# Performance work log

Hardware: AMD Instinct MI355X
Metric: run time of the kernel (lower is better)

Reference implementation:

```python
import jax, jax.numpy as jnp
import numpy as np

N = 20000          # nodes
E = 320000         # edges
D_IN = 128         # input_dim
HGC = 64           # hidden per gconv layer
LG = 4             # number of ChebConv layers
K = 4              # Chebyshev order (hardcoded)
NUM_CLASSES = 2
HID_BYS = 16       # bayesian hidden_dim (hardcoded)
NSAMP = 25         # 5 outer x 5 inner chained sampling iterations
BN_SCALE = 1.0 / np.sqrt(1.0 + 1e-5)  # eval BatchNorm with default running stats
COS_EPS = 1e-8


def setup_inputs() -> dict:
    key = jax.random.key(0)
    ks = jax.random.split(key, 16)
    f32 = jnp.float32
    d = {}
    d["features"] = jax.random.normal(ks[0], (N, D_IN), f32)
    d["edge_index"] = jax.random.randint(ks[1], (2, E), 0, N)
    d["edgenet_input"] = jax.random.normal(ks[2], (E, 128), f32)
    half = 64  # edgenet_input_dim // 2
    # associationP MLP: Linear(64,512) ReLU BN Linear(512,256) ReLU BN Drop Linear(256,128)
    d["We1"] = jax.random.normal(ks[3], (512, half), f32) * np.sqrt(2.0 / half)
    d["be1"] = jnp.zeros((512,), f32)
    d["We2"] = jax.random.normal(ks[4], (256, 512), f32) * np.sqrt(2.0 / 512)
    d["be2"] = jnp.zeros((256,), f32)
    d["We3"] = jax.random.normal(ks[5], (128, 256), f32) * np.sqrt(2.0 / 256)
    d["be3"] = jnp.zeros((128,), f32)
    # ChebConv weights, [K, in, out], no bias
    d["cheb_w0"] = jax.random.normal(ks[6], (K, D_IN, HGC), f32) * np.sqrt(2.0 / D_IN)
    d["cheb_w1"] = jax.random.normal(ks[7], (K, HGC, HGC), f32) * np.sqrt(2.0 / HGC)
    d["cheb_w2"] = jax.random.normal(ks[8], (K, HGC, HGC), f32) * np.sqrt(2.0 / HGC)
    d["cheb_w3"] = jax.random.normal(ks[9], (K, HGC, HGC), f32) * np.sqrt(2.0 / HGC)
    cls_in = HGC * LG  # 256, jumping-knowledge concat
    d["Wm1"] = jax.random.normal(ks[10], (256, cls_in), f32) * np.sqrt(2.0 / cls_in)
    d["bm1"] = jnp.zeros((256,), f32)
    d["Wm2"] = jax.random.normal(ks[11], (NUM_CLASSES, 256), f32) * np.sqrt(2.0 / 256)
    d["bm2"] = jnp.zeros((NUM_CLASSES,), f32)
    d["Wl"] = jax.random.normal(ks[12], (HID_BYS, D_IN), f32) * np.sqrt(2.0 / D_IN)
    d["bl"] = jnp.zeros((HID_BYS,), f32)
    hl_in = NSAMP * HID_BYS  # 400, the freshly-created Linear2
    d["Whl"] = jax.random.normal(ks[13], (NUM_CLASSES, hl_in), f32) * np.sqrt(1.0 / hl_in)
    d["bhl"] = jnp.zeros((NUM_CLASSES,), f32)
    # prior Normal(0,1) samples, one per node per sampling iteration
    d["noise"] = jax.random.normal(ks[14], (NSAMP, N, HID_BYS), f32)
    return d


def _edge_mlp(x, We1, be1, We2, be2, We3, be3):
    h = jax.nn.relu(x @ We1.T + be1) * BN_SCALE
    h = jax.nn.relu(h @ We2.T + be2) * BN_SCALE
    return h @ We3.T + be3


def _forward(features, edge_index, edgenet_input, We1, be1, We2, be2, We3, be3,
             cheb_w0, cheb_w1, cheb_w2, cheb_w3, Wm1, bm1, Wm2, bm2,
             Wl, bl, Whl, bhl, noise):
    row, col = edge_index[0], edge_index[1]

    # ---- edge weights via associationP (cosine similarity head) ----
    h1 = _edge_mlp(edgenet_input[:, :64], We1, be1, We2, be2, We3, be3)
    h2 = _edge_mlp(edgenet_input[:, 64:], We1, be1, We2, be2, We3, be3)
    n1 = jnp.maximum(jnp.sqrt(jnp.sum(h1 * h1, -1)), COS_EPS)
    n2 = jnp.maximum(jnp.sqrt(jnp.sum(h2 * h2, -1)), COS_EPS)
    cos = jnp.sum(h1 * h2, -1) / (n1 * n2)
    ew = (cos + 1.0) * 0.5  # [E]

    # ---- ChebConv sym-normalized scaled Laplacian (lambda_max=2 -> zero diag) ----
    w = jnp.where(row == col, 0.0, ew)  # remove_self_loops
    deg = jax.ops.segment_sum(w, row, num_segments=N)
    dinv = jnp.where(deg > 0, jax.lax.rsqrt(deg), 0.0)
    lapw = -dinv[row] * w * dinv[col]  # L_hat off-diagonal weights

    def prop(x):  # L_hat @ x  (diag is exactly 0)
        return jax.ops.segment_sum(lapw[:, None] * x[row], col, num_segments=N)

    def cheb(x, W):  # W: [K, in, out]
        tx0, tx1 = x, prop(x)
        out = tx0 @ W[0] + tx1 @ W[1]
        for k in range(2, K):
            tx2 = 2.0 * prop(tx1) - tx0
            out = out + tx2 @ W[k]
            tx0, tx1 = tx1, tx2
        return out

    # ---- dense_gcn branch with jumping-knowledge concat ----
    h = jax.nn.relu(cheb(features, cheb_w0))
    jk = h
    for W in (cheb_w1, cheb_w2, cheb_w3):
        h = jax.nn.relu(cheb(h, W))
        jk = jnp.concatenate([jk, h], axis=1)
    m = jax.nn.relu(jk @ Wm1.T + bm1) * BN_SCALE
    logit1 = m @ Wm2.T + bm2  # [N, C]

    # ---- bys_gcn branch: 25 chained iterations h <- noise + scatter_add(w*h[src]) ----
    h0 = features @ Wl.T + bl  # [N, 16]

    def step(hc, nz):
        agg = jax.ops.segment_sum(ew[:, None] * hc[row], col, num_segments=N)
        hn = nz + agg
        return hn, hn

    _, states = jax.lax.scan(step, h0, noise)  # [25, N, 16]
    # faithful to torch .view(N, -1) on the [5,5,N,16] stack (row-major reshape)
    feats2 = states.reshape(N, NSAMP * HID_BYS)  # [N, 400]
    logit2 = jax.nn.sigmoid(feats2 @ Whl.T + bhl)  # [N, C]

    p1 = jax.nn.softmax(logit1, axis=1)
    p2 = jax.nn.softmax(logit2, axis=1)
    return p1, p2, jnp.maximum(p1, p2)


def reference(features, edge_index, edgenet_input, We1, be1, We2, be2, We3, be3,
              cheb_w0, cheb_w1, cheb_w2, cheb_w3, Wm1, bm1, Wm2, bm2,
              Wl, bl, Whl, bhl, noise):
    return _forward(features, edge_index, edgenet_input, We1, be1, We2, be2, We3, be3,
                    cheb_w0, cheb_w1, cheb_w2, cheb_w3, Wm1, bm1, Wm2, bm2,
                    Wl, bl, Whl, bhl, noise)
```

## Files before the change

kernel.cpp:

```cpp
#include <hip/hip_runtime.h>
#include <math.h>

#define NN 20000
#define EE 320000
#define BN_SC 0.9999950000374997f

typedef __attribute__((ext_vector_type(8))) short bf16x8;
typedef __attribute__((ext_vector_type(4))) float f32x4;

__device__ __forceinline__ unsigned short f2b(float x) {
  unsigned int u = __builtin_bit_cast(unsigned int, x);
  u += 0x7FFFu + ((u >> 16) & 1u);
  return (unsigned short)(u >> 16);
}
__device__ __forceinline__ void split2(float x, unsigned short& h, unsigned short& l) {
  h = f2b(x);
  float hf = __builtin_bit_cast(float, (unsigned int)h << 16);
  l = f2b(x - hf);
}

__global__ __launch_bounds__(256) void k_wpack(const float* __restrict__ W, unsigned short* __restrict__ Wh,
                                               unsigned short* __restrict__ Wl, int C, int K) {
  int i = blockIdx.x * 256 + threadIdx.x;
  if (i >= C * K) return;
  int e = i & 7;
  int lane = (i >> 3) & 63;
  int tile = i >> 9;
  int KT = K >> 5;
  int kt = tile % KT, ct = tile / KT;
  int lr = lane & 15, lg = lane >> 4;
  int col = ct * 16 + lr;
  int k = kt * 32 + lg * 8 + e;
  unsigned short h, l;
  split2(W[(size_t)col * K + k], h, l);
  Wh[i] = h;
  Wl[i] = l;
}

__global__ __launch_bounds__(256) void k_count(const int* __restrict__ colv, int* __restrict__ cnt) {
  int e = blockIdx.x * 256 + threadIdx.x;
  if (e < EE) atomicAdd(&cnt[colv[e]], 1);
}

__global__ __launch_bounds__(256) void k_scan1(const int* __restrict__ cnt, int* __restrict__ offs,
                                               int* __restrict__ bsum) {
  __shared__ int sb[256];
  int t = threadIdx.x, i = blockIdx.x * 256 + t;
  int v = (i < NN) ? cnt[i] : 0;
  sb[t] = v;
  __syncthreads();
  for (int off = 1; off < 256; off <<= 1) {
    int x = (t >= off) ? sb[t - off] : 0;
    __syncthreads();
    sb[t] += x;
    __syncthreads();
  }
  if (i < NN) offs[i + 1] = sb[t];
  if (t == 255) bsum[blockIdx.x] = sb[255];
}
__global__ __launch_bounds__(128) void k_scan2(int* __restrict__ bsum) {
  __shared__ int sb[128];
  int t = threadIdx.x;
  int v = (t < 79) ? bsum[t] : 0;
  sb[t] = v;
  __syncthreads();
  for (int off = 1; off < 128; off <<= 1) {
    int x = (t >= off) ? sb[t - off] : 0;
    __syncthreads();
    sb[t] += x;
    __syncthreads();
  }
  if (t < 79) bsum[t] = sb[t] - v;
}
__global__ __launch_bounds__(256) void k_scan3(const int* __restrict__ bsum, int* __restrict__ offs) {
  int i = blockIdx.x * 256 + threadIdx.x;
  if (i == 0) offs[0] = 0;
  if (i < NN) offs[i + 1] += bsum[blockIdx.x];
}

__global__ __launch_bounds__(256) void k_fill(const int* __restrict__ colv, const int* __restrict__ offs,
                                              int* __restrict__ cur, int* __restrict__ eid) {
  int e = blockIdx.x * 256 + threadIdx.x;
  if (e < EE) {
    int d = colv[e];
    int p = atomicAdd(&cur[d], 1);
    eid[offs[d] + p] = e;
  }
}

__global__ __launch_bounds__(64) void k_sortl(const int* __restrict__ offs, int* __restrict__ eid) {
  __shared__ int buf[64 * 97];
  int n = blockIdx.x * 64 + threadIdx.x;
  if (n >= NN) return;
  int j0 = offs[n], j1 = offs[n + 1], d = j1 - j0;
  int* b = &buf[threadIdx.x * 97];
  if (d <= 96) {
    for (int i = 0; i < d; ++i) b[i] = eid[j0 + i];
    for (int i = 1; i < d; ++i) {
      int v = b[i];
      int j = i - 1;
      while (j >= 0 && b[j] > v) { b[j + 1] = b[j]; --j; }
      b[j + 1] = v;
    }
    for (int i = 0; i < d; ++i) eid[j0 + i] = b[i];
  } else {
    for (int i = j0 + 1; i < j1; ++i) {
      int v = eid[i];
      int j = i - 1;
      while (j >= j0 && eid[j] > v) { eid[j + 1] = eid[j]; --j; }
      eid[j + 1] = v;
    }
  }
}

__global__ __launch_bounds__(256) void k_pack(const int* __restrict__ eid, const int* __restrict__ rowi,
                                              const int* __restrict__ colv,
                                              const float* __restrict__ ew, const float* __restrict__ dinv,
                                              float2* __restrict__ packW, float2* __restrict__ packL) {
  int j = blockIdx.x * 256 + threadIdx.x;
  if (j < EE) {
    int e = eid[j];
    int r = rowi[e], c = colv[e];
    float rw = __int_as_float(r);
    float w = (r == c) ? 0.f : ew[e];
    packW[j] = make_float2(ew[e], rw);
    packL[j] = make_float2(-dinv[r] * w * dinv[c], rw);
  }
}

#define MFMA16(a, b, c) __builtin_amdgcn_mfma_f32_16x16x32_bf16(a, b, c, 0, 0, 0)

__global__ __launch_bounds__(512, 2) void k_edge_mlp(
    const float* __restrict__ X,
    const unsigned short* __restrict__ W1h, const unsigned short* __restrict__ W1l, const float* __restrict__ b1,
    const unsigned short* __restrict__ W2h, const unsigned short* __restrict__ W2l, const float* __restrict__ b2,
    const unsigned short* __restrict__ W3h, const unsigned short* __restrict__ W3l, const float* __restrict__ b3,
    float* __restrict__ ew) {
  __shared__ __align__(16) unsigned short POOL[24576];
  unsigned short* Xh = POOL;
  unsigned short* Xl = POOL + 4096;
  unsigned short* H2ch = POOL + 8192;
  unsigned short* H2cl = POOL + 16384;
  float* H3 = (float*)(POOL + 8192);

  const int tid = threadIdx.x;
  const int wv = tid >> 6;
  const int lane = tid & 63;
  const int lr = lane & 15;
  const int lg = lane >> 4;
  const int e0 = blockIdx.x * 32;
  const int lane8 = lane << 3;

  const int rt1 = wv & 3;
  const int ch1 = wv >> 2;

  {
    int row = tid >> 3, eighth = tid & 7;
    const float* src = X + (size_t)(e0 + (row >> 1)) * 128 + (row & 1) * 64 + eighth * 8;
    float4 a = ((const float4*)src)[0];
    float4 b = ((const float4*)src)[1];
    float vals[8] = {a.x, a.y, a.z, a.w, b.x, b.y, b.z, b.w};
    unsigned short hs[8], ls[8];
#pragma unroll
    for (int j = 0; j < 8; ++j) split2(vals[j], hs[j], ls[j]);
    int chunk = eighth ^ (row & 7);
    int idxs = row * 64 + chunk * 8;
#pragma unroll
    for (int j = 0; j < 8; ++j) { Xh[idxs + j] = hs[j]; Xl[idxs + j] = ls[j]; }
  }
  __syncthreads();

  auto l1_compute = [&](int c, int b) {
    unsigned short* H1h = POOL + 8192 + b * 8192;
    unsigned short* H1l = POOL + 12288 + b * 8192;
    f32x4 acc1[2];
#pragma unroll
    for (int cti = 0; cti < 2; ++cti) acc1[cti] = f32x4{0.f, 0.f, 0.f, 0.f};
#pragma unroll
    for (int kt = 0; kt < 2; ++kt) {
      int arow = 16 * rt1 + lr;
      int aidx = arow * 64 + ((4 * kt + lg) ^ (arow & 7)) * 8;
      bf16x8 ah = *(const bf16x8*)&Xh[aidx];
      bf16x8 al = *(const bf16x8*)&Xl[aidx];
#pragma unroll
      for (int cti = 0; cti < 2; ++cti) {
        int off = (((4 * c + 2 * ch1 + cti) * 2 + kt) << 9) + lane8;
        bf16x8 bh = *(const bf16x8*)(W1h + off);
        bf16x8 bl = *(const bf16x8*)(W1l + off);
        acc1[cti] = MFMA16(ah, bh, acc1[cti]);
        acc1[cti] = MFMA16(ah, bl, acc1[cti]);
        acc1[cti] = MFMA16(al, bh, acc1[cti]);
      }
    }
#pragma unroll
    for (int cti = 0; cti < 2; ++cti) {
      int colL = 16 * (2 * ch1 + cti) + lr;
      float bias = b1[64 * c + colL];
#pragma unroll
      for (int r = 0; r < 4; ++r) {
        float v = fmaxf(acc1[cti][r] + bias, 0.f) * BN_SC;
        unsigned short hs, ls;
        split2(v, hs, ls);
        int row = 16 * rt1 + 4 * lg + r;
        int idxs = row * 64 + (((colL >> 3) ^ (row & 7)) * 8) + (colL & 7);
        H1h[idxs] = hs;
        H1l[idxs] = ls;
      }
    }
  };

  f32x4 acc2[4][2];
#pragma unroll
  for (int rt = 0; rt < 4; ++rt)
#pragma unroll
    for (int ct = 0; ct < 2; ++ct) acc2[rt][ct] = f32x4{0.f, 0.f, 0.f, 0.f};

  l1_compute(0, 0);
  __syncthreads();

  for (int kc = 0; kc < 8; ++kc) {
    int cur = kc & 1;
    unsigned short* H1h = POOL + 8192 + cur * 8192;
    unsigned short* H1l = POOL + 12288 + cur * 8192;
    bf16x8 p2h[2], p2l[2];
    {
#pragma unroll
      for (int ct = 0; ct < 2; ++ct) {
        int off = (((8 * ct + wv) * 16 + 2 * kc) << 9) + lane8;
        p2h[ct] = *(const bf16x8*)(W2h + off);
        p2l[ct] = *(const bf16x8*)(W2l + off);
      }
    }
    if (kc < 7) l1_compute(kc + 1, cur ^ 1);
    bf16x8 q2h[2], q2l[2];
    {
#pragma unroll
      for (int ct = 0; ct < 2; ++ct) {
        int off = (((8 * ct + wv) * 16 + 2 * kc + 1) << 9) + lane8;
        q2h[ct] = *(const bf16x8*)(W2h + off);
        q2l[ct] = *(const bf16x8*)(W2l + off);
      }
    }
#pragma unroll
    for (int rtg = 0; rtg < 2; ++rtg) {
      bf16x8 ah[2], al[2];
#pragma unroll
      for (int rti = 0; rti < 2; ++rti) {
        int arow = 32 * rtg + 16 * rti + lr;
        int aidx = arow * 64 + (lg ^ (arow & 7)) * 8;
        ah[rti] = *(const bf16x8*)&H1h[aidx];
        al[rti] = *(const bf16x8*)&H1l[aidx];
      }
#pragma unroll
      for (int ct = 0; ct < 2; ++ct)
#pragma unroll
        for (int rti = 0; rti < 2; ++rti) {
          acc2[2 * rtg + rti][ct] = MFMA16(ah[rti], p2h[ct], acc2[2 * rtg + rti][ct]);
          acc2[2 * rtg + rti][ct] = MFMA16(ah[rti], p2l[ct], acc2[2 * rtg + rti][ct]);
          acc2[2 * rtg + rti][ct] = MFMA16(al[rti], p2h[ct], acc2[2 * rtg + rti][ct]);
        }
    }
#pragma unroll
    for (int rtg = 0; rtg < 2; ++rtg) {
      bf16x8 ah[2], al[2];
#pragma unroll
      for (int rti = 0; rti < 2; ++rti) {
        int arow = 32 * rtg + 16 * rti + lr;
        int aidx = arow * 64 + ((4 + lg) ^ (arow & 7)) * 8;
        ah[rti] = *(const bf16x8*)&H1h[aidx];
        al[rti] = *(const bf16x8*)&H1l[aidx];
      }
#pragma unroll
      for (int ct = 0; ct < 2; ++ct)
#pragma unroll
        for (int rti = 0; rti < 2; ++rti) {
          acc2[2 * rtg + rti][ct] = MFMA16(ah[rti], q2h[ct], acc2[2 * rtg + rti][ct]);
          acc2[2 * rtg + rti][ct] = MFMA16(ah[rti], q2l[ct], acc2[2 * rtg + rti][ct]);
          acc2[2 * rtg + rti][ct] = MFMA16(al[rti], q2h[ct], acc2[2 * rtg + rti][ct]);
        }
    }
    __syncthreads();
  }

  f32x4 acc3[4];
#pragma unroll
  for (int rt = 0; rt < 4; ++rt) acc3[rt] = f32x4{0.f, 0.f, 0.f, 0.f};
  const int w3col = 16 * wv + lr;

#pragma unroll
  for (int ch = 0; ch < 2; ++ch) {
    bf16x8 w3h_c, w3l_c;
    {
      int off = ((wv * 8 + 4 * ch) << 9) + lane8;
      w3h_c = *(const bf16x8*)(W3h + off);
      w3l_c = *(const bf16x8*)(W3l + off);
    }
    if (ch) __syncthreads();
    {
      int colC = 16 * wv + lr;
      float bias = b2[128 * ch + colC];
#pragma unroll
      for (int rt = 0; rt < 4; ++rt) {
#pragma unroll
        for (int r = 0; r < 4; ++r) {
          float v = fmaxf(acc2[rt][ch][r] + bias, 0.f) * BN_SC;
          unsigned short hs, ls;
          split2(v, hs, ls);
          int row = 16 * rt + 4 * lg + r;
          int idxs = row * 128 + (((colC >> 3) ^ (row & 7)) * 8) + (colC & 7);
          H2ch[idxs] = hs;
          H2cl[idxs] = ls;
        }
      }
    }
    __syncthreads();
#pragma unroll
    for (int kt = 0; kt < 4; ++kt) {
      bf16x8 w3h_n, w3l_n;
      if (kt < 3) {
        int off = ((wv * 8 + 4 * ch + kt + 1) << 9) + lane8;
        w3h_n = *(const bf16x8*)(W3h + off);
        w3l_n = *(const bf16x8*)(W3l + off);
      }
#pragma unroll
      for (int rtg = 0; rtg < 2; ++rtg) {
        bf16x8 ah[2], al[2];
#pragma unroll
        for (int rti = 0; rti < 2; ++rti) {
          int arow = 32 * rtg + 16 * rti + lr;
          int aidx = arow * 128 + (((4 * kt + lg) ^ (arow & 7)) * 8);
          ah[rti] = *(const bf16x8*)&H2ch[aidx];
          al[rti] = *(const bf16x8*)&H2cl[aidx];
        }
#pragma unroll
        for (int rti = 0; rti < 2; ++rti) {
          acc3[2 * rtg + rti] = MFMA16(ah[rti], w3h_c, acc3[2 * rtg + rti]);
          acc3[2 * rtg + rti] = MFMA16(ah[rti], w3l_c, acc3[2 * rtg + rti]);
          acc3[2 * rtg + rti] = MFMA16(al[rti], w3h_c, acc3[2 * rtg + rti]);
        }
      }
      w3h_c = w3h_n;
      w3l_c = w3l_n;
    }
  }
  __syncthreads();

  {
    float bias = b3[w3col];
#pragma unroll
    for (int rt = 0; rt < 4; ++rt)
#pragma unroll
      for (int r = 0; r < 4; ++r)
        H3[(16 * rt + 4 * lg + r) * 128 + w3col] = acc3[rt][r] + bias;
  }
  __syncthreads();

  {
    int i = tid >> 4, j = tid & 15;
    const float* ra = &H3[(2 * i) * 128];
    const float* rb = &H3[(2 * i + 1) * 128];
    float dot = 0.f, s1 = 0.f, s2 = 0.f;
#pragma unroll
    for (int s = 0; s < 8; ++s) {
      float a = ra[j + 16 * s], b = rb[j + 16 * s];
      dot += a * b;
      s1 += a * a;
      s2 += b * b;
    }
#pragma unroll
    for (int m = 8; m >= 1; m >>= 1) {
      dot += __shfl_xor(dot, m);
      s1 += __shfl_xor(s1, m);
      s2 += __shfl_xor(s2, m);
    }
    if (j == 0) {
      float n1 = fmaxf(sqrtf(s1), 1e-8f);
      float n2 = fmaxf(sqrtf(s2), 1e-8f);
      float cosv = dot / (n1 * n2);
      ew[e0 + i] = (cosv + 1.f) * 0.5f;
    }
  }
}

__global__ __launch_bounds__(256) void k_deg(const int* __restrict__ rowi, const int* __restrict__ colv,
                                             const float* __restrict__ ew, float* __restrict__ deg) {
  int e = blockIdx.x * 256 + threadIdx.x;
  if (e < EE) {
    int r = rowi[e];
    float w = (r == colv[e]) ? 0.f : ew[e];
    atomicAdd(&deg[r], w);
  }
}
__global__ __launch_bounds__(256) void k_dinv(const float* __restrict__ deg, float* __restrict__ dinv) {
  int n = blockIdx.x * 256 + threadIdx.x;
  if (n < NN) { float d = deg[n]; dinv[n] = d > 0.f ? 1.f / sqrtf(d) : 0.f; }
}

template <int DIM>
__global__ __launch_bounds__(256) void k_prop(const float* __restrict__ x, int ldx,
                                              const float* __restrict__ y, int ldy,
                                              float alpha, float beta,
                                              float* __restrict__ outv, int ldo,
                                              const float2* __restrict__ packL,
                                              const int* __restrict__ offs) {
  constexpr int FG = DIM / 4;
  int idx = blockIdx.x * 256 + threadIdx.x;
  int n = idx / FG, g = (idx % FG) * 4;
  if (n >= NN) return;
  float ax = 0.f, ay = 0.f, az = 0.f, aw = 0.f;
  int j1 = offs[n + 1];
  for (int j = offs[n]; j < j1; ++j) {
    float2 p = packL[j];
    float4 v = *(const float4*)(x + (size_t)__float_as_int(p.y) * ldx + g);
    ax += p.x * v.x; ay += p.x * v.y; az += p.x * v.z; aw += p.x * v.w;
  }
  float4 r = make_float4(alpha * ax, alpha * ay, alpha * az, alpha * aw);
  if (beta != 0.f) {
    float4 yv = *(const float4*)(y + (size_t)n * ldy + g);
    r.x += beta * yv.x; r.y += beta * yv.y; r.z += beta * yv.z; r.w += beta * yv.w;
  }
  *(float4*)(outv + (size_t)n * ldo + g) = r;
}

template <int DK>
__global__ __launch_bounds__(512) void k_combine(const float* __restrict__ t0, int ld0,
                                                 const float* __restrict__ t1, int ld1,
                                                 const float* __restrict__ t2, int ld2,
                                                 const float* __restrict__ t3, int ld3,
                                                 const float* __restrict__ W,
                                                 float* __restrict__ outp) {
  int n = blockIdx.x * 8 + (threadIdx.x >> 6);
  int c = threadIdx.x & 63;
  if (n >= NN) return;
  const float* r0 = t0 + (size_t)n * ld0;
  const float* r1 = t1 + (size_t)n * ld1;
  const float* r2 = t2 + (size_t)n * ld2;
  const float* r3 = t3 + (size_t)n * ld3;
  const float* w0 = W;
  const float* w1 = W + DK * 64;
  const float* w2 = W + 2 * DK * 64;
  const float* w3 = W + 3 * DK * 64;
  float acc = 0.f;
#pragma unroll 4
  for (int d = 0; d < DK; ++d) {
    acc += r0[d] * w0[d * 64 + c];
    acc += r1[d] * w1[d * 64 + c];
    acc += r2[d] * w2[d * 64 + c];
    acc += r3[d] * w3[d * 64 + c];
  }
  outp[(size_t)n * 256 + c] = fmaxf(acc, 0.f);
}

__global__ void k_tr256(const float* __restrict__ A, float* __restrict__ At) {
  int c = blockIdx.x, k = threadIdx.x;
  At[(size_t)k * 256 + c] = A[(size_t)c * 256 + k];
}

__global__ __launch_bounds__(256) void k_mlogit(const float* __restrict__ jk, const float* __restrict__ Wm1t,
                                                const float* __restrict__ bm1, const float* __restrict__ Wm2,
                                                const float* __restrict__ bm2, float* __restrict__ logit1) {
  __shared__ float jks[16 * 256];
  __shared__ float red[16 * 8];
  int tid = threadIdx.x, n0 = blockIdx.x * 16;
  {
    const float4* src = (const float4*)(jk + (size_t)n0 * 256);
    float4* dst = (float4*)jks;
#pragma unroll
    for (int u = 0; u < 4; ++u) dst[tid + 256 * u] = src[tid + 256 * u];
  }
  __syncthreads();
  int c = tid;
  float acc[16];
  float bb = bm1[c];
#pragma unroll
  for (int r = 0; r < 16; ++r) acc[r] = bb;
  for (int k = 0; k < 256; k += 4) {
    float w0 = Wm1t[(size_t)(k + 0) * 256 + c];
    float w1 = Wm1t[(size_t)(k + 1) * 256 + c];
    float w2 = Wm1t[(size_t)(k + 2) * 256 + c];
    float w3 = Wm1t[(size_t)(k + 3) * 256 + c];
#pragma unroll
    for (int r = 0; r < 16; ++r) {
      float4 jv = *(const float4*)&jks[r * 256 + k];
      acc[r] += jv.x * w0 + jv.y * w1 + jv.z * w2 + jv.w * w3;
    }
  }
  float w20 = Wm2[c], w21 = Wm2[256 + c];
  int wid = tid >> 6, lane = tid & 63;
#pragma unroll
  for (int r = 0; r < 16; ++r) {
    float mv = fmaxf(acc[r], 0.f) * BN_SC;
    float v0 = mv * w20, v1 = mv * w21;
#pragma unroll
    for (int m = 32; m >= 1; m >>= 1) {
      v0 += __shfl_xor(v0, m, 64);
      v1 += __shfl_xor(v1, m, 64);
    }
    if (lane == 0) { red[r * 8 + wid] = v0; red[r * 8 + 4 + wid] = v1; }
  }
  __syncthreads();
  if (tid < 32) {
    int r = tid >> 1, cls = tid & 1;
    float s = red[r * 8 + cls * 4] + red[r * 8 + cls * 4 + 1] + red[r * 8 + cls * 4 + 2] + red[r * 8 + cls * 4 + 3];
    logit1[(size_t)(n0 + r) * 2 + cls] = s + bm2[cls];
  }
}

__global__ __launch_bounds__(256) void k_h0(const float* __restrict__ feat, const float* __restrict__ Wl,
                                            const float* __restrict__ bl, float* __restrict__ h0) {
  int idx = blockIdx.x * 256 + threadIdx.x;
  if (idx >= NN * 16) return;
  int n = idx >> 4, j = idx & 15;
  const float* fr = feat + (size_t)n * 128;
  const float* wr = Wl + (size_t)j * 128;
  float acc = bl[j];
#pragma unroll 8
  for (int d = 0; d < 128; d += 4) {
    float4 f = *(const float4*)(fr + d);
    float4 w = *(const float4*)(wr + d);
    acc += f.x * w.x + f.y * w.y + f.z * w.z + f.w * w.w;
  }
  h0[idx] = acc;
}

__global__ __launch_bounds__(256) void k_bys(const float* __restrict__ hprev, const float* __restrict__ nz,
                                             float* __restrict__ hout,
                                             const float2* __restrict__ packW,
                                             const int* __restrict__ offs) {
  int idx = blockIdx.x * 256 + threadIdx.x;
  int n = idx >> 2, g = (idx & 3) * 4;
  if (n >= NN) return;
  float ax = 0.f, ay = 0.f, az = 0.f, aw = 0.f;
  int j1 = offs[n + 1];
  for (int j = offs[n]; j < j1; ++j) {
    float2 p = packW[j];
    float4 v = *(const float4*)(hprev + ((size_t)__float_as_int(p.y) << 4) + g);
    ax += p.x * v.x; ay += p.x * v.y; az += p.x * v.z; aw += p.x * v.w;
  }
  float4 nv = *(const float4*)(nz + ((size_t)n << 4) + g);
  *(float4*)(hout + ((size_t)n << 4) + g) = make_float4(nv.x + ax, nv.y + ay, nv.z + az, nv.w + aw);
}

__global__ __launch_bounds__(256) void k_final(const float* __restrict__ states, const float* __restrict__ Whl,
                                               const float* __restrict__ bhl, const float* __restrict__ logit1,
                                               float* __restrict__ outp) {
  int n = blockIdx.x * 4 + (threadIdx.x >> 6);
  int l = threadIdx.x & 63;
  if (n >= NN) return;
  const float* sf = states + (size_t)n * 400;
  float a0 = 0.f, a1 = 0.f;
  for (int t = l; t < 400; t += 64) {
    float v = sf[t];
    a0 += v * Whl[t];
    a1 += v * Whl[400 + t];
  }
#pragma unroll
  for (int m = 32; m >= 1; m >>= 1) {
    a0 += __shfl_xor(a0, m, 64);
    a1 += __shfl_xor(a1, m, 64);
  }
  if (l == 0) {
    float z0 = 1.f / (1.f + expf(-(a0 + bhl[0])));
    float z1 = 1.f / (1.f + expf(-(a1 + bhl[1])));
    float p20 = 1.f / (1.f + expf(z1 - z0));
    float p21 = 1.f - p20;
    float l10 = logit1[(size_t)n * 2], l11 = logit1[(size_t)n * 2 + 1];
    float p10 = 1.f / (1.f + expf(l11 - l10));
    float p11 = 1.f - p10;
    outp[(size_t)n * 2] = p10;
    outp[(size_t)n * 2 + 1] = p11;
    outp[2 * NN + (size_t)n * 2] = p20;
    outp[2 * NN + (size_t)n * 2 + 1] = p21;
    outp[4 * NN + (size_t)n * 2] = fmaxf(p10, p20);
    outp[4 * NN + (size_t)n * 2 + 1] = fmaxf(p11, p21);
  }
}

extern "C" void kernel_launch(void* const* d_in, const int* in_sizes, int n_in,
                              void* d_out, int out_size, void* d_ws, size_t ws_size,
                              hipStream_t stream) {
  const float* feat = (const float*)d_in[0];
  const int* ei = (const int*)d_in[1];
  const float* xen = (const float*)d_in[2];
  const float* We1 = (const float*)d_in[3];
  const float* be1 = (const float*)d_in[4];
  const float* We2 = (const float*)d_in[5];
  const float* be2 = (const float*)d_in[6];
  const float* We3 = (const float*)d_in[7];
  const float* be3 = (const float*)d_in[8];
  const float* cw[4] = {(const float*)d_in[9], (const float*)d_in[10], (const float*)d_in[11], (const float*)d_in[12]};
  const float* Wm1 = (const float*)d_in[13];
  const float* bm1 = (const float*)d_in[14];
  const float* Wm2 = (const float*)d_in[15];
  const float* bm2 = (const float*)d_in[16];
  const float* Wl = (const float*)d_in[17];
  const float* bl = (const float*)d_in[18];
  const float* Whl = (const float*)d_in[19];
  const float* bhl = (const float*)d_in[20];
  const float* noise = (const float*)d_in[21];
  float* outp = (float*)d_out;

  char* wp_ = (char*)d_ws;
  auto alloc = [&](size_t bytes) {
    char* p = wp_;
    wp_ += (bytes + 255) & ~(size_t)255;
    return p;
  };
  float* ew = (float*)alloc((size_t)EE * 4);
  float* deg = (float*)alloc((size_t)NN * 4);
  float* dinv = (float*)alloc((size_t)NN * 4);
  int* cnt = (int*)alloc((size_t)NN * 4);
  int* offs = (int*)alloc((size_t)(NN + 1) * 4);
  int* bsum = (int*)alloc((size_t)128 * 4);
  int* eid = (int*)alloc((size_t)EE * 4);
  float2* packW = (float2*)alloc((size_t)EE * 8);
  float2* packL = (float2*)alloc((size_t)EE * 8);
  float* tx1 = (float*)alloc((size_t)NN * 128 * 4);
  float* tx2 = (float*)alloc((size_t)NN * 128 * 4);
  float* tx3 = (float*)alloc((size_t)NN * 128 * 4);
  float* jk = (float*)alloc((size_t)NN * 256 * 4);
  float* logit1 = (float*)alloc((size_t)NN * 2 * 4);
  float* Wm1t = (float*)alloc((size_t)256 * 256 * 4);
  float* h0 = (float*)alloc((size_t)NN * 16 * 4);
  float* states = (float*)alloc((size_t)25 * NN * 16 * 4);
  unsigned short* W1h = (unsigned short*)alloc((size_t)32768 * 2);
  unsigned short* W1l = (unsigned short*)alloc((size_t)32768 * 2);
  unsigned short* W2h = (unsigned short*)alloc((size_t)131072 * 2);
  unsigned short* W2l = (unsigned short*)alloc((size_t)131072 * 2);
  unsigned short* W3h = (unsigned short*)alloc((size_t)32768 * 2);
  unsigned short* W3l = (unsigned short*)alloc((size_t)32768 * 2);

  const int* rowi = ei;
  const int* colv = ei + EE;

  k_wpack<<<128, 256, 0, stream>>>(We1, W1h, W1l, 512, 64);
  k_wpack<<<512, 256, 0, stream>>>(We2, W2h, W2l, 256, 512);
  k_wpack<<<128, 256, 0, stream>>>(We3, W3h, W3l, 128, 256);

  hipMemsetAsync(cnt, 0, (size_t)NN * 4, stream);
  hipMemsetAsync(deg, 0, (size_t)NN * 4, stream);
  k_count<<<1250, 256, 0, stream>>>(colv, cnt);
  k_scan1<<<79, 256, 0, stream>>>(cnt, offs, bsum);
  k_scan2<<<1, 128, 0, stream>>>(bsum);
  k_scan3<<<79, 256, 0, stream>>>(bsum, offs);
  hipMemsetAsync(cnt, 0, (size_t)NN * 4, stream);
  k_fill<<<1250, 256, 0, stream>>>(colv, offs, cnt, eid);
  k_sortl<<<313, 64, 0, stream>>>(offs, eid);

  k_edge_mlp<<<10000, 512, 0, stream>>>(xen, W1h, W1l, be1, W2h, W2l, be2, W3h, W3l, be3, ew);

  k_deg<<<1250, 256, 0, stream>>>(rowi, colv, ew, deg);
  k_dinv<<<79, 256, 0, stream>>>(deg, dinv);
  k_pack<<<1250, 256, 0, stream>>>(eid, rowi, colv, ew, dinv, packW, packL);
  k_tr256<<<256, 256, 0, stream>>>(Wm1, Wm1t);

  k_prop<128><<<2500, 256, 0, stream>>>(feat, 128, feat, 128, 1.f, 0.f, tx1, 128, packL, offs);
  k_prop<128><<<2500, 256, 0, stream>>>(tx1, 128, feat, 128, 2.f, -1.f, tx2, 128, packL, offs);
  k_prop<128><<<2500, 256, 0, stream>>>(tx2, 128, tx1, 128, 2.f, -1.f, tx3, 128, packL, offs);
  k_combine<128><<<2500, 512, 0, stream>>>(feat, 128, tx1, 128, tx2, 128, tx3, 128, cw[0], jk);
  for (int l = 1; l < 4; ++l) {
    const float* xin = jk + (l - 1) * 64;
    k_prop<64><<<1250, 256, 0, stream>>>(xin, 256, xin, 256, 1.f, 0.f, tx1, 64, packL, offs);
    k_prop<64><<<1250, 256, 0, stream>>>(tx1, 64, xin, 256, 2.f, -1.f, tx2, 64, packL, offs);
    k_prop<64><<<1250, 256, 0, stream>>>(tx2, 64, tx1, 64, 2.f, -1.f, tx3, 64, packL, offs);
    k_combine<64><<<2500, 512, 0, stream>>>(xin, 256, tx1, 64, tx2, 64, tx3, 64, cw[l], jk + l * 64);
  }
  k_mlogit<<<1250, 256, 0, stream>>>(jk, Wm1t, bm1, Wm2, bm2, logit1);

  k_h0<<<1250, 256, 0, stream>>>(feat, Wl, bl, h0);
  const float* hprev = h0;
  for (int s = 0; s < 25; ++s) {
    float* hout = states + (size_t)s * NN * 16;
    k_bys<<<313, 256, 0, stream>>>(hprev, noise + (size_t)s * NN * 16, hout, packW, offs);
    hprev = hout;
  }
  k_final<<<5000, 256, 0, stream>>>(states, Whl, bhl, logit1, outp);
}
```

Before: 1.812 ms.

## Fuse h0 projection and 25 bys propagation steps into one persistent kernel with grid barriers

The 26 separate launches (the h0 projection plus 25 chained scatter steps) are replaced by one persistent kernel of 313 blocks that computes h0 and then loops over the 25 steps, separated by a software grid barrier built from atomics and threadfences. The aim is to remove per-launch overhead and the idle gaps between the small dependent launches. The h0 computation is rewritten so that each thread produces 4 outputs instead of 1. This relies on all 313 blocks being co-resident, otherwise the barrier deadlocks. Each step now pays for the barrier's atomic traffic and fences.

Result: slower. 3.553 ms (+96.1%).

```diff
diff --git a/kernel.cpp b/kernel.cpp
--- a/kernel.cpp
+++ b/kernel.cpp
@@ -4,6 +4,7 @@
 #define NN 20000
 #define EE 320000
 #define BN_SC 0.9999950000374997f
+#define BYS_NB 313
 
 typedef __attribute__((ext_vector_type(8))) short bf16x8;
 typedef __attribute__((ext_vector_type(4))) float f32x4;
@@ -506,39 +507,64 @@
   }
 }
 
-__global__ __launch_bounds__(256) void k_h0(const float* __restrict__ feat, const float* __restrict__ Wl,
-                                            const float* __restrict__ bl, float* __restrict__ h0) {
-  int idx = blockIdx.x * 256 + threadIdx.x;
-  if (idx >= NN * 16) return;
-  int n = idx >> 4, j = idx & 15;
-  const float* fr = feat + (size_t)n * 128;
-  const float* wr = Wl + (size_t)j * 128;
-  float acc = bl[j];
-#pragma unroll 8
-  for (int d = 0; d < 128; d += 4) {
-    float4 f = *(const float4*)(fr + d);
-    float4 w = *(const float4*)(wr + d);
-    acc += f.x * w.x + f.y * w.y + f.z * w.z + f.w * w.w;
-  }
-  h0[idx] = acc;
-}
-
-__global__ __launch_bounds__(256) void k_bys(const float* __restrict__ hprev, const float* __restrict__ nz,
-                                             float* __restrict__ hout,
-                                             const float2* __restrict__ packW,
-                                             const int* __restrict__ offs) {
+__device__ __forceinline__ void gridbar(int* __restrict__ bar, int nb) {
+  __threadfence();
+  __syncthreads();
+  if (threadIdx.x == 0) {
+    int g = atomicAdd(bar + 1, 0);
+    if (atomicAdd(bar, 1) == nb - 1) {
+      atomicExch(bar, 0);
+      __threadfence();
+      atomicAdd(bar + 1, 1);
+    } else {
+      while (atomicAdd(bar + 1, 0) == g) __builtin_amdgcn_s_sleep(8);
+    }
+  }
+  __syncthreads();
+  __threadfence();
+}
+
+__global__ __launch_bounds__(256) void k_bys_all(
+    const float* __restrict__ feat, const float* __restrict__ Wl, const float* __restrict__ bl,
+    const float* __restrict__ noise, float* __restrict__ states, float* __restrict__ h0buf,
+    const float2* __restrict__ packW, const int* __restrict__ offs, int* __restrict__ bar) {
   int idx = blockIdx.x * 256 + threadIdx.x;
   int n = idx >> 2, g = (idx & 3) * 4;
-  if (n >= NN) return;
-  float ax = 0.f, ay = 0.f, az = 0.f, aw = 0.f;
-  int j1 = offs[n + 1];
-  for (int j = offs[n]; j < j1; ++j) {
-    float2 p = packW[j];
-    float4 v = *(const float4*)(hprev + ((size_t)__float_as_int(p.y) << 4) + g);
-    ax += p.x * v.x; ay += p.x * v.y; az += p.x * v.z; aw += p.x * v.w;
-  }
-  float4 nv = *(const float4*)(nz + ((size_t)n << 4) + g);
-  *(float4*)(hout + ((size_t)n << 4) + g) = make_float4(nv.x + ax, nv.y + ay, nv.z + az, nv.w + aw);
+  if (n < NN) {
+    const float* fr = feat + (size_t)n * 128;
+    float a0 = bl[g], a1 = bl[g + 1], a2 = bl[g + 2], a3 = bl[g + 3];
+    for (int d = 0; d < 128; d += 4) {
+      float4 f = *(const float4*)(fr + d);
+      float4 w0 = *(const float4*)(Wl + (size_t)g * 128 + d);
+      float4 w1 = *(const float4*)(Wl + (size_t)(g + 1) * 128 + d);
+      float4 w2 = *(const float4*)(Wl + (size_t)(g + 2) * 128 + d);
+      float4 w3 = *(const float4*)(Wl + (size_t)(g + 3) * 128 + d);
+      a0 += f.x * w0.x + f.y * w0.y + f.z * w0.z + f.w * w0.w;
+      a1 += f.x * w1.x + f.y * w1.y + f.z * w1.z + f.w * w1.w;
+      a2 += f.x * w2.x + f.y * w2.y + f.z * w2.z + f.w * w2.w;
+      a3 += f.x * w3.x + f.y * w3.y + f.z * w3.z + f.w * w3.w;
+    }
+    *(float4*)(h0buf + ((size_t)n << 4) + g) = make_float4(a0, a1, a2, a3);
+  }
+  const float* hprev = h0buf;
+  int j0 = (n < NN) ? offs[n] : 0;
+  int j1 = (n < NN) ? offs[n + 1] : 0;
+  for (int s = 0; s < 25; ++s) {
+    gridbar(bar, BYS_NB);
+    float* hout = states + (size_t)s * NN * 16;
+    if (n < NN) {
+      float ax = 0.f, ay = 0.f, az = 0.f, aw = 0.f;
+      for (int j = j0; j < j1; ++j) {
+        float2 p = packW[j];
+        float4 v = *(const float4*)(hprev + ((size_t)__float_as_int(p.y) << 4) + g);
+        ax += p.x * v.x; ay += p.x * v.y; az += p.x * v.z; aw += p.x * v.w;
+      }
+      const float* nz = noise + (size_t)s * NN * 16;
+      float4 nv = *(const float4*)(nz + ((size_t)n << 4) + g);
+      *(float4*)(hout + ((size_t)n << 4) + g) = make_float4(nv.x + ax, nv.y + ay, nv.z + az, nv.w + aw);
+    }
+    hprev = hout;
+  }
 }
 
 __global__ __launch_bounds__(256) void k_final(const float* __restrict__ states, const float* __restrict__ Whl,
@@ -612,6 +638,7 @@
   int* cnt = (int*)alloc((size_t)NN * 4);
   int* offs = (int*)alloc((size_t)(NN + 1) * 4);
   int* bsum = (int*)alloc((size_t)128 * 4);
+  int* bar = (int*)alloc((size_t)256);
   int* eid = (int*)alloc((size_t)EE * 4);
   float2* packW = (float2*)alloc((size_t)EE * 8);
   float2* packL = (float2*)alloc((size_t)EE * 8);
@@ -639,6 +666,7 @@
 
   hipMemsetAsync(cnt, 0, (size_t)NN * 4, stream);
   hipMemsetAsync(deg, 0, (size_t)NN * 4, stream);
+  hipMemsetAsync(bar, 0, 256, stream);
   k_count<<<1250, 256, 0, stream>>>(colv, cnt);
   k_scan1<<<79, 256, 0, stream>>>(cnt, offs, bsum);
   k_scan2<<<1, 128, 0, stream>>>(bsum);
@@ -667,12 +695,6 @@
   }
   k_mlogit<<<1250, 256, 0, stream>>>(jk, Wm1t, bm1, Wm2, bm2, logit1);
 
-  k_h0<<<1250, 256, 0, stream>>>(feat, Wl, bl, h0);
-  const float* hprev = h0;
-  for (int s = 0; s < 25; ++s) {
-    float* hout = states + (size_t)s * NN * 16;
-    k_bys<<<313, 256, 0, stream>>>(hprev, noise + (size_t)s * NN * 16, hout, packW, offs);
-    hprev = hout;
-  }
+  k_bys_all<<<BYS_NB, 256, 0, stream>>>(feat, Wl, bl, noise, states, h0, packW, offs, bar);
   k_final<<<5000, 256, 0, stream>>>(states, Whl, bhl, logit1, outp);
 }
```
